# Performance work log

Hardware: AMD Instinct MI355X
Metric: run time of the kernel (lower is better)

## Reference

```python
import jax, jax.numpy as jnp
import numpy as np

B, S, D = 4, 4096, 64
D_MODEL = 64


def setup_inputs() -> dict:
    key = jax.random.key(0)
    kq, kk, kv, km = jax.random.split(key, 4)
    q = jax.random.normal(kq, (B, S, D), dtype=jnp.float32)
    k = jax.random.normal(kk, (B, S, D), dtype=jnp.float32)
    v = jax.random.normal(kv, (B, S, D), dtype=jnp.float32)
    mask = jax.random.uniform(km, (B, S, S), dtype=jnp.float32)
    return {"q": q, "k": k, "v": v, "mask": mask}


def reference(q, k, v, mask):
    dk = jnp.sqrt(jnp.asarray(D_MODEL, dtype=q.dtype))
    # [B,S,S] scores; multiplicative (non-additive) mask applied pre-softmax
    scaled_qk = jnp.einsum('bqd,bkd->bqk', q, k) / dk
    scaled_qk = scaled_qk * mask
    attn = jax.nn.softmax(scaled_qk, axis=-1)
    return jnp.einsum('bqk,bkd->bqd', attn, v)
```

## Files before the change

### kernel.cpp

```cpp
#include <hip/hip_runtime.h>
#include <hip/hip_bf16.h>

#define S_LEN 4096
#define DH 64
#define NBATCH 4

typedef __attribute__((ext_vector_type(8))) short bf16x8;
typedef __attribute__((ext_vector_type(4))) short bf16x4;
typedef __attribute__((ext_vector_type(4))) float f32x4;

static __device__ __forceinline__ short f2bf(float x) {
  __hip_bfloat16 h = __float2bfloat16(x);
  return *reinterpret_cast<short*>(&h);
}

#define MFMA(a, b, c) __builtin_amdgcn_mfma_f32_16x16x32_bf16((a), (b), (c), 0, 0, 0)

__global__ __launch_bounds__(256) void cvt_qk_kernel(const float* __restrict__ q,
                                                     const float* __restrict__ k,
                                                     short* __restrict__ qb,
                                                     short* __restrict__ kb) {
  int i = (blockIdx.x * 256 + threadIdx.x) * 4;
  f32x4 xq = *(const f32x4*)(q + i);
  f32x4 xk = *(const f32x4*)(k + i);
  bf16x4 oq, ok;
#pragma unroll
  for (int j = 0; j < 4; ++j) { oq[j] = f2bf(xq[j]); ok[j] = f2bf(xk[j]); }
  *(bf16x4*)(qb + i) = oq;
  *(bf16x4*)(kb + i) = ok;
}

__global__ __launch_bounds__(256) void cvt_vT_kernel(const float* __restrict__ v,
                                                     short* __restrict__ vt) {
  __shared__ float tile[64][65];
  const int t = threadIdx.x;
  const int b = blockIdx.x >> 6;
  const int s0 = (blockIdx.x & 63) << 6;
#pragma unroll
  for (int p = 0; p < 4; ++p) {
    const int r = p * 16 + (t >> 4);
    const int c = (t & 15) * 4;
    const f32x4 x = *(const f32x4*)(v + (size_t)(b * S_LEN + s0 + r) * DH + c);
    tile[r][c] = x[0]; tile[r][c + 1] = x[1]; tile[r][c + 2] = x[2]; tile[r][c + 3] = x[3];
  }
  __syncthreads();
  const int d = t >> 2;
  const int sc = (t & 3) * 16;
  bf16x8 o0, o1;
#pragma unroll
  for (int j = 0; j < 8; ++j) {
    o0[j] = f2bf(tile[sc + j][d]);
    o1[j] = f2bf(tile[sc + 8 + j][d]);
  }
  short* dst = vt + (((size_t)(b * DH + d)) << 12) + s0 + sc;
  *(bf16x8*)dst = o0;
  *((bf16x8*)(dst + 8)) = o1;
}

__global__ __launch_bounds__(256, 4) void fa_kernel(
    const short* __restrict__ qb, const short* __restrict__ kb,
    const short* __restrict__ vt, const float* __restrict__ mask,
    float* __restrict__ out) {
  __shared__ __align__(16) short lds_p[4][16][40];
  __shared__ float lds_O[4][16][64];
  __shared__ float lds_l[4][16];

  const int tid = threadIdx.x;
  const int w = tid >> 6;
  const int lane = tid & 63;
  const int quad = lane >> 4;
  const int n16 = lane & 15;

  const int b = blockIdx.x >> 8;
  const int q0 = (blockIdx.x & 255) << 4;

  const short* qrow = qb + (size_t)(b * S_LEN + q0 + n16) * DH;
  const bf16x8 aQ0 = *(const bf16x8*)(qrow + quad * 8);
  const bf16x8 aQ1 = *(const bf16x8*)(qrow + 32 + quad * 8);

  f32x4 O0 = {0.f, 0.f, 0.f, 0.f}, O1 = O0, O2 = O0, O3 = O0;
  float lacc[4] = {0.f, 0.f, 0.f, 0.f};

  const float* mrow0 = mask + ((size_t)b * S_LEN + q0 + quad * 4) * S_LEN;
  const short* kbb = kb + (size_t)b * S_LEN * DH;
  const short* vbase = vt + (((size_t)(b * DH)) << 12);

  float mA[8], mB[8];

#define LOAD_MASK(DST, KK)                                   \
  {                                                          \
    const int kk_ = (KK);                                    \
    _Pragma("unroll") for (int r = 0; r < 4; ++r) {          \
      DST[r]     = mrow0[(size_t)r * S_LEN + kk_ + n16];     \
      DST[4 + r] = mrow0[(size_t)r * S_LEN + kk_ + 16 + n16];\
    }                                                        \
  }

#define FA_STEP(MREG, K0)                                                  \
  {                                                                        \
    const int k0_ = (K0);                                                  \
    const short* kr = kbb + (k0_ + n16) * DH;                              \
    const bf16x8 bk0 = *(const bf16x8*)(kr + quad * 8);                    \
    const bf16x8 bk1 = *(const bf16x8*)(kr + 32 + quad * 8);               \
    const bf16x8 bk2 = *(const bf16x8*)(kr + 16 * DH + quad * 8);          \
    const bf16x8 bk3 = *(const bf16x8*)(kr + 16 * DH + 32 + quad * 8);     \
    const short* vp = vbase + k0_ + quad * 8 + (((size_t)n16) << 12);      \
    const bf16x8 v0 = *(const bf16x8*)(vp);                                \
    const bf16x8 v1 = *(const bf16x8*)(vp + (16 << 12));                   \
    const bf16x8 v2 = *(const bf16x8*)(vp + (32 << 12));                   \
    const bf16x8 v3 = *(const bf16x8*)(vp + (48 << 12));                   \
    const f32x4 z = {0.f, 0.f, 0.f, 0.f};                                  \
    f32x4 s0 = MFMA(aQ0, bk0, z); s0 = MFMA(aQ1, bk1, s0);                 \
    f32x4 s1 = MFMA(aQ0, bk2, z); s1 = MFMA(aQ1, bk3, s1);                 \
    _Pragma("unroll") for (int r = 0; r < 4; ++r) {                        \
      float p0 = __expf(s0[r] * 0.125f * MREG[r]);                         \
      float p1 = __expf(s1[r] * 0.125f * MREG[4 + r]);                     \
      lacc[r] += p0 + p1;                                                  \
      lds_p[w][quad * 4 + r][n16] = f2bf(p0);                              \
      lds_p[w][quad * 4 + r][16 + n16] = f2bf(p1);                         \
    }                                                                      \
    const bf16x8 aP = *(const bf16x8*)(&lds_p[w][n16][quad * 8]);          \
    O0 = MFMA(aP, v0, O0); O1 = MFMA(aP, v1, O1);                          \
    O2 = MFMA(aP, v2, O2); O3 = MFMA(aP, v3, O3);                          \
  }

  LOAD_MASK(mA, w * 32);
  LOAD_MASK(mB, 128 + w * 32);

  for (int it = 0; it < 16; ++it) {
    const int k0 = it * 256 + w * 32;
    FA_STEP(mA, k0);
    LOAD_MASK(mA, (k0 + 256) & (S_LEN - 1));
    FA_STEP(mB, k0 + 128);
    LOAD_MASK(mB, (k0 + 384) & (S_LEN - 1));
  }
#undef LOAD_MASK
#undef FA_STEP

#pragma unroll
  for (int r = 0; r < 4; ++r) {
#pragma unroll
    for (int off = 1; off < 16; off <<= 1) lacc[r] += __shfl_xor(lacc[r], off);
  }

#pragma unroll
  for (int r = 0; r < 4; ++r) {
    int row = quad * 4 + r;
    lds_O[w][row][n16]      = O0[r];
    lds_O[w][row][16 + n16] = O1[r];
    lds_O[w][row][32 + n16] = O2[r];
    lds_O[w][row][48 + n16] = O3[r];
    if (n16 == 0) lds_l[w][row] = lacc[r];
  }
  __syncthreads();

  const int r = tid >> 4;
  const int c = (tid & 15) << 2;
  const float linv =
      1.0f / (lds_l[0][r] + lds_l[1][r] + lds_l[2][r] + lds_l[3][r]);
  f32x4 o;
#pragma unroll
  for (int j = 0; j < 4; ++j)
    o[j] = (lds_O[0][r][c + j] + lds_O[1][r][c + j] + lds_O[2][r][c + j] +
            lds_O[3][r][c + j]) *
           linv;
  *(f32x4*)(out + (size_t)(b * S_LEN + q0 + r) * DH + c) = o;
}

extern "C" void kernel_launch(void* const* d_in, const int* in_sizes, int n_in,
                              void* d_out, int out_size, void* d_ws, size_t ws_size,
                              hipStream_t stream) {
  const float* q = (const float*)d_in[0];
  const float* k = (const float*)d_in[1];
  const float* v = (const float*)d_in[2];
  const float* mask = (const float*)d_in[3];
  float* out = (float*)d_out;

  short* qb = (short*)d_ws;
  short* kb = qb + (size_t)NBATCH * S_LEN * DH;
  short* vt = kb + (size_t)NBATCH * S_LEN * DH;

  cvt_qk_kernel<<<(NBATCH * S_LEN * DH) / (256 * 4), 256, 0, stream>>>(q, k, qb, kb);
  cvt_vT_kernel<<<NBATCH * (S_LEN / 64), 256, 0, stream>>>(v, vt);
  fa_kernel<<<NBATCH * (S_LEN / 16), 256, 0, stream>>>(qb, kb, vt, mask, out);
}
```

Measured before the change: 449.5 us.

## Split key range across two blocks and pre-swizzle K/V into MFMA fragment layout

The key dimension is split in half so each query tile is handled by two blocks. This doubles the grid and raises occupancy (launch bounds go from 4 to 6). Partial outputs and row sums are combined with atomicAdd into a zeroed output, and a separate normalization kernel divides by the summed row sums afterwards. K and V are also pre-packed into per-lane MFMA fragment order so each lane reads contiguous 16-byte chunks instead of strided rows. This adds memsets, atomics and an extra pass over the output.

```diff
diff --git a/kernel.cpp b/kernel.cpp
--- a/kernel.cpp
+++ b/kernel.cpp
@@ -16,51 +16,60 @@
 
 #define MFMA(a, b, c) __builtin_amdgcn_mfma_f32_16x16x32_bf16((a), (b), (c), 0, 0, 0)
 
-__global__ __launch_bounds__(256) void cvt_qk_kernel(const float* __restrict__ q,
-                                                     const float* __restrict__ k,
-                                                     short* __restrict__ qb,
-                                                     short* __restrict__ kb) {
+__global__ __launch_bounds__(256) void cvt_q_kernel(const float* __restrict__ q,
+                                                    short* __restrict__ qb) {
   int i = (blockIdx.x * 256 + threadIdx.x) * 4;
-  f32x4 xq = *(const f32x4*)(q + i);
-  f32x4 xk = *(const f32x4*)(k + i);
-  bf16x4 oq, ok;
-#pragma unroll
-  for (int j = 0; j < 4; ++j) { oq[j] = f2bf(xq[j]); ok[j] = f2bf(xk[j]); }
-  *(bf16x4*)(qb + i) = oq;
-  *(bf16x4*)(kb + i) = ok;
-}
-
-__global__ __launch_bounds__(256) void cvt_vT_kernel(const float* __restrict__ v,
-                                                     short* __restrict__ vt) {
-  __shared__ float tile[64][65];
+  f32x4 x = *(const f32x4*)(q + i);
+  bf16x4 o;
+#pragma unroll
+  for (int j = 0; j < 4; ++j) o[j] = f2bf(x[j]);
+  *(bf16x4*)(qb + i) = o;
+}
+
+__global__ __launch_bounds__(256) void cvt_frag_kernel(const float* __restrict__ k,
+                                                       const float* __restrict__ v,
+                                                       short* __restrict__ kfrag,
+                                                       short* __restrict__ vfrag) {
+  __shared__ short kt[32][80];
+  __shared__ short vt[32][80];
   const int t = threadIdx.x;
-  const int b = blockIdx.x >> 6;
-  const int s0 = (blockIdx.x & 63) << 6;
-#pragma unroll
-  for (int p = 0; p < 4; ++p) {
-    const int r = p * 16 + (t >> 4);
-    const int c = (t & 15) * 4;
-    const f32x4 x = *(const f32x4*)(v + (size_t)(b * S_LEN + s0 + r) * DH + c);
-    tile[r][c] = x[0]; tile[r][c + 1] = x[1]; tile[r][c + 2] = x[2]; tile[r][c + 3] = x[3];
+  const int b = blockIdx.x >> 7;
+  const int i = blockIdx.x & 127;
+  const size_t src0 = ((size_t)b * S_LEN + i * 32) * DH;
+  {
+    const int row = t >> 3, c0 = (t & 7) * 8;
+    const f32x4 xk0 = *(const f32x4*)(k + src0 + row * DH + c0);
+    const f32x4 xk1 = *(const f32x4*)(k + src0 + row * DH + c0 + 4);
+    const f32x4 xv0 = *(const f32x4*)(v + src0 + row * DH + c0);
+    const f32x4 xv1 = *(const f32x4*)(v + src0 + row * DH + c0 + 4);
+#pragma unroll
+    for (int j = 0; j < 4; ++j) {
+      kt[row][c0 + j] = f2bf(xk0[j]);  kt[row][c0 + 4 + j] = f2bf(xk1[j]);
+      vt[row][c0 + j] = f2bf(xv0[j]);  vt[row][c0 + 4 + j] = f2bf(xv1[j]);
+    }
   }
   __syncthreads();
-  const int d = t >> 2;
-  const int sc = (t & 3) * 16;
-  bf16x8 o0, o1;
-#pragma unroll
-  for (int j = 0; j < 8; ++j) {
-    o0[j] = f2bf(tile[sc + j][d]);
-    o1[j] = f2bf(tile[sc + 8 + j][d]);
-  }
-  short* dst = vt + (((size_t)(b * DH + d)) << 12) + s0 + sc;
-  *(bf16x8*)dst = o0;
-  *((bf16x8*)(dst + 8)) = o1;
-}
-
-__global__ __launch_bounds__(256, 4) void fa_kernel(
-    const short* __restrict__ qb, const short* __restrict__ kb,
-    const short* __restrict__ vt, const float* __restrict__ mask,
-    float* __restrict__ out) {
+  const int c = t >> 6, l = t & 63;
+  const size_t dst = (((size_t)(b * 128 + i) * 4 + c) * 64 + l) * 8;
+  {
+    const int kr = ((c >> 1) * 16) + (l & 15);
+    const int d0 = ((c & 1) * 32) + (l >> 4) * 8;
+    *(bf16x8*)(kfrag + dst) = *(const bf16x8*)&kt[kr][d0];
+  }
+  {
+    bf16x8 f;
+    const int col = c * 16 + (l & 15);
+    const int r0 = (l >> 4) * 8;
+#pragma unroll
+    for (int j = 0; j < 8; ++j) f[j] = vt[r0 + j][col];
+    *(bf16x8*)(vfrag + dst) = f;
+  }
+}
+
+__global__ __launch_bounds__(256, 6) void fa_kernel(
+    const short* __restrict__ qb, const short* __restrict__ kfrag,
+    const short* __restrict__ vfrag, const float* __restrict__ mask,
+    float* __restrict__ out, float* __restrict__ lsum) {
   __shared__ __align__(16) short lds_p[4][16][40];
   __shared__ float lds_O[4][16][64];
   __shared__ float lds_l[4][16];
@@ -71,8 +80,10 @@
   const int quad = lane >> 4;
   const int n16 = lane & 15;
 
-  const int b = blockIdx.x >> 8;
-  const int q0 = (blockIdx.x & 255) << 4;
+  const int b = blockIdx.x >> 9;
+  const int rest = blockIdx.x & 511;
+  const int q0 = (rest >> 1) << 4;
+  const int hh = rest & 1;
 
   const short* qrow = qb + (size_t)(b * S_LEN + q0 + n16) * DH;
   const bf16x8 aQ0 = *(const bf16x8*)(qrow + quad * 8);
@@ -81,34 +92,34 @@
   f32x4 O0 = {0.f, 0.f, 0.f, 0.f}, O1 = O0, O2 = O0, O3 = O0;
   float lacc[4] = {0.f, 0.f, 0.f, 0.f};
 
-  const float* mrow0 = mask + ((size_t)b * S_LEN + q0 + quad * 4) * S_LEN;
-  const short* kbb = kb + (size_t)b * S_LEN * DH;
-  const short* vbase = vt + (((size_t)(b * DH)) << 12);
+  const float* mrow0 =
+      mask + ((size_t)b * S_LEN + q0 + quad * 4) * S_LEN + hh * 2048;
+  const short* kfb = kfrag + ((size_t)(b * 128 + hh * 64 + w) * 2048);
+  const short* vfb = vfrag + ((size_t)(b * 128 + hh * 64 + w) * 2048);
 
   float mA[8], mB[8];
 
-#define LOAD_MASK(DST, KK)                                   \
-  {                                                          \
-    const int kk_ = (KK);                                    \
-    _Pragma("unroll") for (int r = 0; r < 4; ++r) {          \
-      DST[r]     = mrow0[(size_t)r * S_LEN + kk_ + n16];     \
-      DST[4 + r] = mrow0[(size_t)r * S_LEN + kk_ + 16 + n16];\
-    }                                                        \
-  }
-
-#define FA_STEP(MREG, K0)                                                  \
+#define LOAD_MASK(DST, LK)                                    \
+  {                                                           \
+    const int lk_ = (LK);                                     \
+    _Pragma("unroll") for (int r = 0; r < 4; ++r) {           \
+      DST[r]     = mrow0[(size_t)r * S_LEN + lk_ + n16];      \
+      DST[4 + r] = mrow0[(size_t)r * S_LEN + lk_ + 16 + n16]; \
+    }                                                         \
+  }
+
+#define FA_STEP(MREG, SS)                                                  \
   {                                                                        \
-    const int k0_ = (K0);                                                  \
-    const short* kr = kbb + (k0_ + n16) * DH;                              \
-    const bf16x8 bk0 = *(const bf16x8*)(kr + quad * 8);                    \
-    const bf16x8 bk1 = *(const bf16x8*)(kr + 32 + quad * 8);               \
-    const bf16x8 bk2 = *(const bf16x8*)(kr + 16 * DH + quad * 8);          \
-    const bf16x8 bk3 = *(const bf16x8*)(kr + 16 * DH + 32 + quad * 8);     \
-    const short* vp = vbase + k0_ + quad * 8 + (((size_t)n16) << 12);      \
-    const bf16x8 v0 = *(const bf16x8*)(vp);                                \
-    const bf16x8 v1 = *(const bf16x8*)(vp + (16 << 12));                   \
-    const bf16x8 v2 = *(const bf16x8*)(vp + (32 << 12));                   \
-    const bf16x8 v3 = *(const bf16x8*)(vp + (48 << 12));                   \
+    const short* kf = kfb + (SS) * 8192;                                   \
+    const bf16x8 bk0 = *(const bf16x8*)(kf + lane * 8);                    \
+    const bf16x8 bk1 = *(const bf16x8*)(kf + 512 + lane * 8);              \
+    const bf16x8 bk2 = *(const bf16x8*)(kf + 1024 + lane * 8);             \
+    const bf16x8 bk3 = *(const bf16x8*)(kf + 1536 + lane * 8);             \
+    const short* vf = vfb + (SS) * 8192;                                   \
+    const bf16x8 v0 = *(const bf16x8*)(vf + lane * 8);                     \
+    const bf16x8 v1 = *(const bf16x8*)(vf + 512 + lane * 8);               \
+    const bf16x8 v2 = *(const bf16x8*)(vf + 1024 + lane * 8);              \
+    const bf16x8 v3 = *(const bf16x8*)(vf + 1536 + lane * 8);              \
     const f32x4 z = {0.f, 0.f, 0.f, 0.f};                                  \
     f32x4 s0 = MFMA(aQ0, bk0, z); s0 = MFMA(aQ1, bk1, s0);                 \
     f32x4 s1 = MFMA(aQ0, bk2, z); s1 = MFMA(aQ1, bk3, s1);                 \
@@ -127,12 +138,12 @@
   LOAD_MASK(mA, w * 32);
   LOAD_MASK(mB, 128 + w * 32);
 
-  for (int it = 0; it < 16; ++it) {
-    const int k0 = it * 256 + w * 32;
-    FA_STEP(mA, k0);
-    LOAD_MASK(mA, (k0 + 256) & (S_LEN - 1));
-    FA_STEP(mB, k0 + 128);
-    LOAD_MASK(mB, (k0 + 384) & (S_LEN - 1));
+  for (int it = 0; it < 8; ++it) {
+    const int s2 = it * 2;
+    FA_STEP(mA, s2);
+    LOAD_MASK(mA, ((s2 + 2) * 128 + w * 32) & 2047);
+    FA_STEP(mB, s2 + 1);
+    LOAD_MASK(mB, ((s2 + 3) * 128 + w * 32) & 2047);
   }
 #undef LOAD_MASK
 #undef FA_STEP
@@ -155,16 +166,25 @@
   __syncthreads();
 
   const int r = tid >> 4;
-  const int c = (tid & 15) << 2;
-  const float linv =
-      1.0f / (lds_l[0][r] + lds_l[1][r] + lds_l[2][r] + lds_l[3][r]);
-  f32x4 o;
+  const int c4 = (tid & 15) << 2;
+  float* op = out + (size_t)(b * S_LEN + q0 + r) * DH + c4;
 #pragma unroll
   for (int j = 0; j < 4; ++j)
-    o[j] = (lds_O[0][r][c + j] + lds_O[1][r][c + j] + lds_O[2][r][c + j] +
-            lds_O[3][r][c + j]) *
-           linv;
-  *(f32x4*)(out + (size_t)(b * S_LEN + q0 + r) * DH + c) = o;
+    atomicAdd(op + j, lds_O[0][r][c4 + j] + lds_O[1][r][c4 + j] +
+                          lds_O[2][r][c4 + j] + lds_O[3][r][c4 + j]);
+  if (tid < 16)
+    atomicAdd(lsum + (size_t)b * S_LEN + q0 + tid,
+              lds_l[0][tid] + lds_l[1][tid] + lds_l[2][tid] + lds_l[3][tid]);
+}
+
+__global__ __launch_bounds__(256) void norm_kernel(float* __restrict__ out,
+                                                   const float* __restrict__ lsum) {
+  int i = (blockIdx.x * 256 + threadIdx.x) * 4;
+  f32x4 x = *(f32x4*)(out + i);
+  const float inv = 1.0f / lsum[i >> 6];
+#pragma unroll
+  for (int j = 0; j < 4; ++j) x[j] *= inv;
+  *(f32x4*)(out + i) = x;
 }
 
 extern "C" void kernel_launch(void* const* d_in, const int* in_sizes, int n_in,
@@ -177,10 +197,15 @@
   float* out = (float*)d_out;
 
   short* qb = (short*)d_ws;
-  short* kb = qb + (size_t)NBATCH * S_LEN * DH;
-  short* vt = kb + (size_t)NBATCH * S_LEN * DH;
-
-  cvt_qk_kernel<<<(NBATCH * S_LEN * DH) / (256 * 4), 256, 0, stream>>>(q, k, qb, kb);
-  cvt_vT_kernel<<<NBATCH * (S_LEN / 64), 256, 0, stream>>>(v, vt);
-  fa_kernel<<<NBATCH * (S_LEN / 16), 256, 0, stream>>>(qb, kb, vt, mask, out);
-}
+  short* kfrag = qb + (size_t)NBATCH * S_LEN * DH;
+  short* vfrag = kfrag + (size_t)NBATCH * S_LEN * DH;
+  float* lsum = (float*)(vfrag + (size_t)NBATCH * S_LEN * DH);
+
+  hipMemsetAsync(d_out, 0, (size_t)NBATCH * S_LEN * DH * sizeof(float), stream);
+  hipMemsetAsync(lsum, 0, (size_t)NBATCH * S_LEN * sizeof(float), stream);
+
+  cvt_q_kernel<<<(NBATCH * S_LEN * DH) / 1024, 256, 0, stream>>>(q, qb);
+  cvt_frag_kernel<<<NBATCH * 128, 256, 0, stream>>>(k, v, kfrag, vfrag);
+  fa_kernel<<<NBATCH * 512, 256, 0, stream>>>(qb, kfrag, vfrag, mask, out, lsum);
+  norm_kernel<<<(NBATCH * S_LEN * DH) / 1024, 256, 0, stream>>>(out, lsum);
+}
```

New measurement: 431.8 us. 1.04x faster.
